# Performance work log

Hardware: AMD Instinct MI355X
Metric: run time of the kernel (lower is better)

## Reference

```python
import jax, jax.numpy as jnp
import numpy as np

B, N, F_IN, F_OUT, T, E = 2, 50000, 2, 32, 12, 800000


def _uniform(k, shape, scale):
    return jax.random.uniform(k, shape, jnp.float32, -scale, scale)


def setup_inputs() -> dict:
    key = jax.random.key(0)
    ks = jax.random.split(key, 18)
    inp = {
        "X": jax.random.normal(ks[0], (B, N, F_IN, T), dtype=jnp.float32),
        "edge_index": jax.random.randint(ks[1], (2, E), 0, N, dtype=jnp.int64),
        "edge_weight": jax.random.uniform(ks[2], (E,), dtype=jnp.float32),
    }
    # GCNConv weights [F_IN, F_OUT] (glorot) + bias, for gates z, r, h
    g = float(np.sqrt(6.0 / (F_IN + F_OUT)))
    inp["Wz"] = _uniform(ks[3], (F_IN, F_OUT), g); inp["bz"] = jnp.zeros((F_OUT,), jnp.float32)
    inp["Wr"] = _uniform(ks[4], (F_IN, F_OUT), g); inp["br"] = jnp.zeros((F_OUT,), jnp.float32)
    inp["Wh"] = _uniform(ks[5], (F_IN, F_OUT), g); inp["bh"] = jnp.zeros((F_OUT,), jnp.float32)
    # Linear(2*F_OUT -> F_OUT) per gate (stored as [2*F_OUT, F_OUT] for x @ W)
    l = float(np.sqrt(1.0 / (2 * F_OUT)))
    inp["Lz_w"] = _uniform(ks[6], (2 * F_OUT, F_OUT), l); inp["Lz_b"] = _uniform(ks[7], (F_OUT,), l)
    inp["Lr_w"] = _uniform(ks[8], (2 * F_OUT, F_OUT), l); inp["Lr_b"] = _uniform(ks[9], (F_OUT,), l)
    inp["Lh_w"] = _uniform(ks[10], (2 * F_OUT, F_OUT), l); inp["Lh_b"] = _uniform(ks[11], (F_OUT,), l)
    # attention logits over periods, init uniform(0,1)
    inp["attention"] = jax.random.uniform(ks[12], (T,), dtype=jnp.float32)
    return inp


def _a3tgcn(X, edge_index, edge_weight, Wz, bz, Wr, br, Wh, bh,
            Lz_w, Lz_b, Lr_w, Lr_b, Lh_w, Lh_b, attention):
    n = X.shape[1]
    loop = jnp.arange(n)
    row = jnp.concatenate([edge_index[0], loop])  # sources (+ self loops)
    col = jnp.concatenate([edge_index[1], loop])  # targets
    w = jnp.concatenate([edge_weight, jnp.ones((n,), X.dtype)])
    deg = jax.ops.segment_sum(w, col, num_segments=n)
    dinv = jnp.where(deg > 0, jax.lax.rsqrt(deg), 0.0)
    norm = dinv[row] * w * dinv[col]  # [E+N] sym-normalized coeffs

    def gcn(x, W, b):
        xw = jnp.einsum('bnf,fo->bno', x, W)                # [B,N,O]
        msg = xw[:, row, :] * norm[None, :, None]           # [B,E+N,O]
        agg = jax.vmap(lambda m: jax.ops.segment_sum(m, col, num_segments=n))(msg)
        return agg + b

    probs = jax.nn.softmax(attention)
    H0 = jnp.zeros((X.shape[0], n, Wz.shape[1]), X.dtype)

    def step(carry, inputs):
        H, acc = carry
        Xt, p = inputs  # Xt: [B,N,F_IN]
        Z = jax.nn.sigmoid(jnp.concatenate([gcn(Xt, Wz, bz), H], -1) @ Lz_w + Lz_b)
        R = jax.nn.sigmoid(jnp.concatenate([gcn(Xt, Wr, br), H], -1) @ Lr_w + Lr_b)
        Ht = jnp.tanh(jnp.concatenate([gcn(Xt, Wh, bh), H * R], -1) @ Lh_w + Lh_b)
        Hn = Z * H + (1.0 - Z) * Ht
        return (Hn, acc + p * Hn), None

    xs = jnp.moveaxis(X, -1, 0)  # [T,B,N,F_IN]
    (_, H_accum), _ = jax.lax.scan(step, (H0, H0), (xs, probs))
    return H_accum


def reference(X, edge_index, edge_weight, Wz, bz, Wr, br, Wh, bh,
              Lz_w, Lz_b, Lr_w, Lr_b, Lh_w, Lh_b, attention):
    return _a3tgcn(X, edge_index, edge_weight, Wz, bz, Wr, br, Wh, bh,
                   Lz_w, Lz_b, Lr_w, Lr_b, Lh_w, Lh_b, attention)
```

## Files before the change

kernel.cpp:

```cpp
#include <hip/hip_runtime.h>

#define NN 50000
#define EE 800000
#define TT 12
#define BB 2

#define OFF_AX   50048
#define OFF_P    2450048
#define OFF_CNT  2454144
#define OFF_OFF  2504192
#define OFF_CUR  2554240
#define OFF_BSUM 2604288
#define NB_SCAN  98
#define NPAIR    (BB * NN / 2)
#define NW       4
#define NBLK_REC 1563

__device__ __forceinline__ float fsig(float x) {
    x = fminf(fmaxf(x, -30.f), 30.f);
    return __builtin_amdgcn_rcpf(1.f + __expf(-x));
}
__device__ __forceinline__ float ftanh(float x) {
    x = fminf(fmaxf(x, -15.f), 15.f);
    float e = __expf(-2.f * x);
    return (1.f - e) * __builtin_amdgcn_rcpf(1.f + e);
}

__global__ void k_zero(int* __restrict__ cnt) {
    int i = blockIdx.x * 256 + threadIdx.x;
    if (i < NN) cnt[i] = 0;
}

__global__ void k_count(const int* __restrict__ idx, int* __restrict__ cnt) {
    int e = blockIdx.x * 256 + threadIdx.x;
    if (e < EE) atomicAdd(&cnt[idx[EE + e]], 1);
}

__global__ void k_scanA(const int* __restrict__ cnt, int* __restrict__ off,
                        int* __restrict__ bsum) {
    __shared__ int sm[512];
    int i = blockIdx.x * 512 + threadIdx.x;
    int v = (i < NN) ? cnt[i] : 0;
    sm[threadIdx.x] = v;
    __syncthreads();
#pragma unroll
    for (int d = 1; d < 512; d <<= 1) {
        int t = (threadIdx.x >= d) ? sm[threadIdx.x - d] : 0;
        __syncthreads();
        sm[threadIdx.x] += t;
        __syncthreads();
    }
    if (i < NN) off[i] = sm[threadIdx.x] - v;
    if (threadIdx.x == 511) bsum[blockIdx.x] = sm[511];
}

__global__ void k_scanB(int* __restrict__ bsum) {
    __shared__ int sm[128];
    int tid = threadIdx.x;
    int v = (tid < NB_SCAN) ? bsum[tid] : 0;
    sm[tid] = v;
    __syncthreads();
#pragma unroll
    for (int d = 1; d < 128; d <<= 1) {
        int t = (tid >= d) ? sm[tid - d] : 0;
        __syncthreads();
        sm[tid] += t;
        __syncthreads();
    }
    if (tid < NB_SCAN) bsum[tid] = sm[tid] - v;
}

__global__ void k_scanC(int* __restrict__ off, const int* __restrict__ bsum,
                        int* __restrict__ cur) {
    int i = blockIdx.x * 256 + threadIdx.x;
    if (i < NN) {
        int o = off[i] + bsum[i >> 9];
        off[i] = o;
        cur[i] = o;
    }
}

__global__ void k_fill(const int* __restrict__ idx, const float* __restrict__ w,
                       int* __restrict__ cur, int* __restrict__ esrc,
                       float* __restrict__ ewgt) {
    int e = blockIdx.x * 256 + threadIdx.x;
    if (e >= EE) return;
    int c = idx[EE + e];
    int s = atomicAdd(&cur[c], 1);
    esrc[s] = idx[e];
    ewgt[s] = w[e];
}

__global__ void k_degdinv(const int* __restrict__ off, const int* __restrict__ cnt,
                          const float* __restrict__ ewgt, float* __restrict__ dinv) {
    int n = blockIdx.x * 256 + threadIdx.x;
    if (n >= NN) return;
    int s0 = off[n], c = cnt[n];
    float d = 1.f;
    for (int q = 0; q < c; q++) d += ewgt[s0 + q];
    dinv[n] = rsqrtf(d);
}

__global__ __launch_bounds__(256) void k_gather(const float* __restrict__ X,
                                                const float* __restrict__ dinv,
                                                const int* __restrict__ esrc,
                                                const float* __restrict__ ewgt,
                                                const int* __restrict__ off,
                                                const int* __restrict__ cnt,
                                                float* __restrict__ AX) {
    int tid = blockIdx.x * 256 + threadIdx.x;
    if (tid >= BB * NN) return;
    int b = tid / NN;
    int n = tid - b * NN;
    float di = dinv[n];
    const float* Xb = X + (size_t)b * NN * 24;

    float xf[24], acc[24];
    {
        const float4* xs = (const float4*)(Xb + (size_t)n * 24);
        float s = di * di;
#pragma unroll
        for (int q = 0; q < 6; q++) {
            float4 v = xs[q];
            xf[4 * q] = v.x; xf[4 * q + 1] = v.y; xf[4 * q + 2] = v.z; xf[4 * q + 3] = v.w;
        }
#pragma unroll
        for (int t = 0; t < TT; t++) {
            acc[2 * t] = s * xf[t];
            acc[2 * t + 1] = s * xf[12 + t];
        }
    }
    int s0 = off[n], c = cnt[n];
    for (int q = 0; q < c; q++) {
        int r = esrc[s0 + q];
        float nrm = dinv[r] * ewgt[s0 + q] * di;
        const float4* xr = (const float4*)(Xb + (size_t)r * 24);
#pragma unroll
        for (int p = 0; p < 6; p++) {
            float4 v = xr[p];
            xf[4 * p] = v.x; xf[4 * p + 1] = v.y; xf[4 * p + 2] = v.z; xf[4 * p + 3] = v.w;
        }
#pragma unroll
        for (int t = 0; t < TT; t++) {
            acc[2 * t] = fmaf(nrm, xf[t], acc[2 * t]);
            acc[2 * t + 1] = fmaf(nrm, xf[12 + t], acc[2 * t + 1]);
        }
    }
    float4* o = (float4*)(AX + (size_t)tid * 24);
#pragma unroll
    for (int q = 0; q < 6; q++)
        o[q] = make_float4(acc[4 * q], acc[4 * q + 1], acc[4 * q + 2], acc[4 * q + 3]);
}

__global__ void k_fold(const float* __restrict__ Wz, const float* __restrict__ bz,
                       const float* __restrict__ Lwz, const float* __restrict__ Lbz,
                       const float* __restrict__ Wr, const float* __restrict__ br,
                       const float* __restrict__ Lwr, const float* __restrict__ Lbr,
                       const float* __restrict__ Wh, const float* __restrict__ bh,
                       const float* __restrict__ Lwh, const float* __restrict__ Lbh,
                       const float* __restrict__ att, float* __restrict__ P) {
    int tid = threadIdx.x;
    if (tid < 96) {
        int g = tid >> 5, j = tid & 31;
        const float* W  = g == 0 ? Wz  : (g == 1 ? Wr  : Wh);
        const float* b  = g == 0 ? bz  : (g == 1 ? br  : bh);
        const float* Lw = g == 0 ? Lwz : (g == 1 ? Lwr : Lwh);
        const float* Lb = g == 0 ? Lbz : (g == 1 ? Lbr : Lbh);
        float* out = P + g * 1120;
        float w0 = 0.f, w1 = 0.f, c = 0.f;
        for (int k = 0; k < 32; k++) {
            float lw = Lw[k * 32 + j];
            w0 += W[k] * lw;
            w1 += W[32 + k] * lw;
            c  += b[k] * lw;
        }
        out[j] = w0;
        out[32 + j] = w1;
        out[64 + j] = c + Lb[j];
        for (int k = 0; k < 32; k++) out[96 + k * 32 + j] = Lw[(32 + k) * 32 + j];
    } else if (tid == 96) {
        float m = -1e30f;
        for (int t = 0; t < TT; t++) m = fmaxf(m, att[t]);
        float s = 0.f;
        float e[TT];
        for (int t = 0; t < TT; t++) { e[t] = __expf(att[t] - m); s += e[t]; }
        for (int t = 0; t < TT; t++) P[3360 + t] = e[t] / s;
    }
}

__global__ __launch_bounds__(256) void k_recur(const float* __restrict__ AX,
                                               const float* __restrict__ P,
                                               float* __restrict__ out) {
    __shared__ __align__(16) float Hs[NW][2][32];
    __shared__ __align__(16) float rHs[NW][2][32];
    __shared__ __align__(16) float AXs[NW][2][24];
    const int lane = threadIdx.x & 63;
    const int w = threadIdx.x >> 6;
    const int j = lane & 31;
    const int grp = lane >> 5;
    const int gwave = blockIdx.x * NW + w;

    float LBz[32], LBr[32], LBh[32];
    float wz0 = P[j],        wz1 = P[32 + j],        cz = P[64 + j];
    float wr0 = P[1120 + j], wr1 = P[1120 + 32 + j], cr = P[1120 + 64 + j];
    float wh0 = P[2240 + j], wh1 = P[2240 + 32 + j], ch = P[2240 + 64 + j];
#pragma unroll
    for (int k = 0; k < 32; k++) {
        LBz[k] = P[96 + k * 32 + j];
        LBr[k] = P[1120 + 96 + k * 32 + j];
        LBh[k] = P[2240 + 96 + k * 32 + j];
    }

#pragma unroll 1
    for (int p = gwave; p < NPAIR; p += NBLK_REC * NW) {
        int node = p * 2 + grp;
        if (j < 24) AXs[w][grp][j] = AX[(size_t)node * 24 + j];

        float2 a = *(const float2*)&AXs[w][grp][0];
        float z = fsig(fmaf(a.x, wz0, fmaf(a.y, wz1, cz)));
        float th = ftanh(fmaf(a.x, wh0, fmaf(a.y, wh1, ch)));
        float H = (1.f - z) * th;
        float acc = P[3360] * H;
        Hs[w][grp][j] = H;

#pragma unroll 1
        for (int t = 1; t < TT; t++) {
            a = *(const float2*)&AXs[w][grp][2 * t];
            float hb[32];
#pragma unroll
            for (int i = 0; i < 8; i++) {
                float4 v = *(const float4*)&Hs[w][grp][4 * i];
                hb[4 * i] = v.x; hb[4 * i + 1] = v.y;
                hb[4 * i + 2] = v.z; hb[4 * i + 3] = v.w;
            }
            float r;
            {
                float s0 = 0.f, s1 = 0.f, s2 = 0.f, s3 = 0.f;
#pragma unroll
                for (int k = 0; k < 32; k += 4) {
                    s0 = fmaf(hb[k],     LBr[k],     s0);
                    s1 = fmaf(hb[k + 1], LBr[k + 1], s1);
                    s2 = fmaf(hb[k + 2], LBr[k + 2], s2);
                    s3 = fmaf(hb[k + 3], LBr[k + 3], s3);
                }
                r = fmaf(a.x, wr0, fmaf(a.y, wr1, cr)) + ((s0 + s1) + (s2 + s3));
            }
            rHs[w][grp][j] = fsig(r) * H;
            {
                float s0 = 0.f, s1 = 0.f, s2 = 0.f, s3 = 0.f;
#pragma unroll
                for (int k = 0; k < 32; k += 4) {
                    s0 = fmaf(hb[k],     LBz[k],     s0);
                    s1 = fmaf(hb[k + 1], LBz[k + 1], s1);
                    s2 = fmaf(hb[k + 2], LBz[k + 2], s2);
                    s3 = fmaf(hb[k + 3], LBz[k + 3], s3);
                }
                z = fsig(fmaf(a.x, wz0, fmaf(a.y, wz1, cz)) + ((s0 + s1) + (s2 + s3)));
            }
            float rb[32];
#pragma unroll
            for (int i = 0; i < 8; i++) {
                float4 v = *(const float4*)&rHs[w][grp][4 * i];
                rb[4 * i] = v.x; rb[4 * i + 1] = v.y;
                rb[4 * i + 2] = v.z; rb[4 * i + 3] = v.w;
            }
            {
                float s0 = 0.f, s1 = 0.f, s2 = 0.f, s3 = 0.f;
#pragma unroll
                for (int k = 0; k < 32; k += 4) {
                    s0 = fmaf(rb[k],     LBh[k],     s0);
                    s1 = fmaf(rb[k + 1], LBh[k + 1], s1);
                    s2 = fmaf(rb[k + 2], LBh[k + 2], s2);
                    s3 = fmaf(rb[k + 3], LBh[k + 3], s3);
                }
                th = ftanh(fmaf(a.x, wh0, fmaf(a.y, wh1, ch)) + ((s0 + s1) + (s2 + s3)));
            }
            float Hn = fmaf(z, H - th, th);
            H = Hn;
            acc = fmaf(P[3360 + t], Hn, acc);
            Hs[w][grp][j] = Hn;
        }
        out[(size_t)node * 32 + j] = acc;
    }
}

extern "C" void kernel_launch(void* const* d_in, const int* in_sizes, int n_in,
                              void* d_out, int out_size, void* d_ws, size_t ws_size,
                              hipStream_t stream) {
    const float* X   = (const float*)d_in[0];
    const int*   idx = (const int*)d_in[1];
    const float* ew  = (const float*)d_in[2];
    const float* Wz  = (const float*)d_in[3];
    const float* bz  = (const float*)d_in[4];
    const float* Wr  = (const float*)d_in[5];
    const float* br  = (const float*)d_in[6];
    const float* Wh  = (const float*)d_in[7];
    const float* bh  = (const float*)d_in[8];
    const float* Lwz = (const float*)d_in[9];
    const float* Lbz = (const float*)d_in[10];
    const float* Lwr = (const float*)d_in[11];
    const float* Lbr = (const float*)d_in[12];
    const float* Lwh = (const float*)d_in[13];
    const float* Lbh = (const float*)d_in[14];
    const float* att = (const float*)d_in[15];

    float* ws   = (float*)d_ws;
    float* dinv = ws;
    float* AX   = ws + OFF_AX;
    float* P    = ws + OFF_P;
    int*   cnt  = (int*)ws + OFF_CNT;
    int*   off  = (int*)ws + OFF_OFF;
    int*   cur  = (int*)ws + OFF_CUR;
    int*   bsum = (int*)ws + OFF_BSUM;
    float* out  = (float*)d_out;
    int*   esrc = (int*)d_out;
    float* ewgt = (float*)d_out + EE;

    hipLaunchKernelGGL(k_zero, dim3((NN + 255) / 256), dim3(256), 0, stream, cnt);
    hipLaunchKernelGGL(k_count, dim3((EE + 255) / 256), dim3(256), 0, stream, idx, cnt);
    hipLaunchKernelGGL(k_scanA, dim3(NB_SCAN), dim3(512), 0, stream, cnt, off, bsum);
    hipLaunchKernelGGL(k_scanB, dim3(1), dim3(128), 0, stream, bsum);
    hipLaunchKernelGGL(k_scanC, dim3((NN + 255) / 256), dim3(256), 0, stream, off, bsum, cur);
    hipLaunchKernelGGL(k_fill, dim3((EE + 255) / 256), dim3(256), 0, stream, idx, ew, cur, esrc, ewgt);
    hipLaunchKernelGGL(k_degdinv, dim3((NN + 255) / 256), dim3(256), 0, stream, off, cnt, ewgt, dinv);
    hipLaunchKernelGGL(k_gather, dim3((BB * NN + 255) / 256), dim3(256), 0, stream,
                       X, dinv, esrc, ewgt, off, cnt, AX);
    hipLaunchKernelGGL(k_fold, dim3(1), dim3(128), 0, stream,
                       Wz, bz, Lwz, Lbz, Wr, br, Lwr, Lbr, Wh, bh, Lwh, Lbh, att, P);
    hipLaunchKernelGGL(k_recur, dim3(NBLK_REC), dim3(256), 0, stream, AX, P, out);
}
```

Before: 335.7 us.

## Split recurrence matvec K-dimension across half-waves with shuffle reduction

```diff
diff --git a/kernel.cpp b/kernel.cpp
--- a/kernel.cpp
+++ b/kernel.cpp
@@ -12,7 +12,7 @@
 #define OFF_CUR  2554240
 #define OFF_BSUM 2604288
 #define NB_SCAN  98
-#define NPAIR    (BB * NN / 2)
+#define NNODES   (BB * NN)
 #define NW       4
 #define NBLK_REC 1563
 
@@ -109,7 +109,7 @@
                                                 const int* __restrict__ cnt,
                                                 float* __restrict__ AX) {
     int tid = blockIdx.x * 256 + threadIdx.x;
-    if (tid >= BB * NN) return;
+    if (tid >= NNODES) return;
     int b = tid / NN;
     int n = tid - b * NN;
     float di = dinv[n];
@@ -191,96 +191,104 @@
 __global__ __launch_bounds__(256) void k_recur(const float* __restrict__ AX,
                                                const float* __restrict__ P,
                                                float* __restrict__ out) {
-    __shared__ __align__(16) float Hs[NW][2][32];
-    __shared__ __align__(16) float rHs[NW][2][32];
-    __shared__ __align__(16) float AXs[NW][2][24];
+    __shared__ __align__(16) float Hs[NW][32];
+    __shared__ __align__(16) float rHs[NW][32];
+    __shared__ __align__(16) float AXs[NW][24];
     const int lane = threadIdx.x & 63;
     const int w = threadIdx.x >> 6;
     const int j = lane & 31;
-    const int grp = lane >> 5;
+    const int h = lane >> 5;
+    const int k0 = h * 16;
     const int gwave = blockIdx.x * NW + w;
 
-    float LBz[32], LBr[32], LBh[32];
+    float LBz[16], LBr[16], LBh[16];
     float wz0 = P[j],        wz1 = P[32 + j],        cz = P[64 + j];
     float wr0 = P[1120 + j], wr1 = P[1120 + 32 + j], cr = P[1120 + 64 + j];
     float wh0 = P[2240 + j], wh1 = P[2240 + 32 + j], ch = P[2240 + 64 + j];
 #pragma unroll
-    for (int k = 0; k < 32; k++) {
-        LBz[k] = P[96 + k * 32 + j];
-        LBr[k] = P[1120 + 96 + k * 32 + j];
-        LBh[k] = P[2240 + 96 + k * 32 + j];
+    for (int k = 0; k < 16; k++) {
+        LBz[k] = P[96 + (k0 + k) * 32 + j];
+        LBr[k] = P[1120 + 96 + (k0 + k) * 32 + j];
+        LBh[k] = P[2240 + 96 + (k0 + k) * 32 + j];
     }
 
 #pragma unroll 1
-    for (int p = gwave; p < NPAIR; p += NBLK_REC * NW) {
-        int node = p * 2 + grp;
-        if (j < 24) AXs[w][grp][j] = AX[(size_t)node * 24 + j];
-
-        float2 a = *(const float2*)&AXs[w][grp][0];
+    for (int node = gwave; node < NNODES; node += NBLK_REC * NW) {
+        if (lane < 24) AXs[w][lane] = AX[(size_t)node * 24 + lane];
+
+        float2 a = *(const float2*)&AXs[w][0];
         float z = fsig(fmaf(a.x, wz0, fmaf(a.y, wz1, cz)));
         float th = ftanh(fmaf(a.x, wh0, fmaf(a.y, wh1, ch)));
         float H = (1.f - z) * th;
         float acc = P[3360] * H;
-        Hs[w][grp][j] = H;
+        if (lane < 32) Hs[w][j] = H;
 
 #pragma unroll 1
         for (int t = 1; t < TT; t++) {
-            a = *(const float2*)&AXs[w][grp][2 * t];
-            float hb[32];
-#pragma unroll
-            for (int i = 0; i < 8; i++) {
-                float4 v = *(const float4*)&Hs[w][grp][4 * i];
+            a = *(const float2*)&AXs[w][2 * t];
+            float hb[16];
+#pragma unroll
+            for (int i = 0; i < 4; i++) {
+                float4 v = *(const float4*)&Hs[w][k0 + 4 * i];
                 hb[4 * i] = v.x; hb[4 * i + 1] = v.y;
                 hb[4 * i + 2] = v.z; hb[4 * i + 3] = v.w;
             }
-            float r;
+            float sr;
             {
                 float s0 = 0.f, s1 = 0.f, s2 = 0.f, s3 = 0.f;
 #pragma unroll
-                for (int k = 0; k < 32; k += 4) {
+                for (int k = 0; k < 16; k += 4) {
                     s0 = fmaf(hb[k],     LBr[k],     s0);
                     s1 = fmaf(hb[k + 1], LBr[k + 1], s1);
                     s2 = fmaf(hb[k + 2], LBr[k + 2], s2);
                     s3 = fmaf(hb[k + 3], LBr[k + 3], s3);
                 }
-                r = fmaf(a.x, wr0, fmaf(a.y, wr1, cr)) + ((s0 + s1) + (s2 + s3));
-            }
-            rHs[w][grp][j] = fsig(r) * H;
+                sr = (s0 + s1) + (s2 + s3);
+            }
+            sr += __shfl_xor(sr, 32, 64);
+            float rH = fsig(fmaf(a.x, wr0, fmaf(a.y, wr1, cr)) + sr) * H;
+            if (lane < 32) rHs[w][j] = rH;
+            float sz;
             {
                 float s0 = 0.f, s1 = 0.f, s2 = 0.f, s3 = 0.f;
 #pragma unroll
-                for (int k = 0; k < 32; k += 4) {
+                for (int k = 0; k < 16; k += 4) {
                     s0 = fmaf(hb[k],     LBz[k],     s0);
                     s1 = fmaf(hb[k + 1], LBz[k + 1], s1);
                     s2 = fmaf(hb[k + 2], LBz[k + 2], s2);
                     s3 = fmaf(hb[k + 3], LBz[k + 3], s3);
                 }
-                z = fsig(fmaf(a.x, wz0, fmaf(a.y, wz1, cz)) + ((s0 + s1) + (s2 + s3)));
-            }
-            float rb[32];
-#pragma unroll
-            for (int i = 0; i < 8; i++) {
-                float4 v = *(const float4*)&rHs[w][grp][4 * i];
+                sz = (s0 + s1) + (s2 + s3);
+            }
+            sz += __shfl_xor(sz, 32, 64);
+            z = fsig(fmaf(a.x, wz0, fmaf(a.y, wz1, cz)) + sz);
+            float rb[16];
+#pragma unroll
+            for (int i = 0; i < 4; i++) {
+                float4 v = *(const float4*)&rHs[w][k0 + 4 * i];
                 rb[4 * i] = v.x; rb[4 * i + 1] = v.y;
                 rb[4 * i + 2] = v.z; rb[4 * i + 3] = v.w;
             }
+            float sh;
             {
                 float s0 = 0.f, s1 = 0.f, s2 = 0.f, s3 = 0.f;
 #pragma unroll
-                for (int k = 0; k < 32; k += 4) {
+                for (int k = 0; k < 16; k += 4) {
                     s0 = fmaf(rb[k],     LBh[k],     s0);
                     s1 = fmaf(rb[k + 1], LBh[k + 1], s1);
                     s2 = fmaf(rb[k + 2], LBh[k + 2], s2);
                     s3 = fmaf(rb[k + 3], LBh[k + 3], s3);
                 }
-                th = ftanh(fmaf(a.x, wh0, fmaf(a.y, wh1, ch)) + ((s0 + s1) + (s2 + s3)));
-            }
+                sh = (s0 + s1) + (s2 + s3);
+            }
+            sh += __shfl_xor(sh, 32, 64);
+            th = ftanh(fmaf(a.x, wh0, fmaf(a.y, wh1, ch)) + sh);
             float Hn = fmaf(z, H - th, th);
             H = Hn;
             acc = fmaf(P[3360 + t], Hn, acc);
-            Hs[w][grp][j] = Hn;
-        }
-        out[(size_t)node * 32 + j] = acc;
+            if (lane < 32 && t < TT - 1) Hs[w][j] = Hn;
+        }
+        if (lane < 32) out[(size_t)node * 32 + j] = acc;
     }
 }
 
@@ -323,7 +331,7 @@
     hipLaunchKernelGGL(k_scanC, dim3((NN + 255) / 256), dim3(256), 0, stream, off, bsum, cur);
     hipLaunchKernelGGL(k_fill, dim3((EE + 255) / 256), dim3(256), 0, stream, idx, ew, cur, esrc, ewgt);
     hipLaunchKernelGGL(k_degdinv, dim3((NN + 255) / 256), dim3(256), 0, stream, off, cnt, ewgt, dinv);
-    hipLaunchKernelGGL(k_gather, dim3((BB * NN + 255) / 256), dim3(256), 0, stream,
+    hipLaunchKernelGGL(k_gather, dim3((NNODES + 255) / 256), dim3(256), 0, stream,
                        X, dinv, esrc, ewgt, off, cnt, AX);
     hipLaunchKernelGGL(k_fold, dim3(1), dim3(128), 0, stream,
                        Wz, bz, Lwz, Lbz, Wr, br, Lwr, Lbr, Wh, bh, Lwh, Lbh, att, P);
```

New measurement: 370.3 us. +10.3%, slower.
